# Kernel optimization log

Measured on AMD Instinct MI355X. Metric: run time of the kernel, lower is better.

## Reference

```python
import jax, jax.numpy as jnp
import numpy as np

N_II = 100000      # item nodes
N_UIU = 200000     # user + item nodes
D = 64             # embedding_dim
E_II = 600000
E_UIU = 1200000
L_II = 3           # num_layers_ii
L_UIU = 3          # num_layers_uiu
N_USERS = 100000   # items occupy indices [N_USERS, N_USERS+N_II)


def _lightgcn_embedding(x, edge_index, edge_weight, num_layers, num_nodes):
    """PyG LightGCN.get_embedding: symmetric gcn_norm (no self loops) + mean over layer outputs."""
    src, dst = edge_index[0], edge_index[1]
    # gcn_norm: deg over target nodes, weighted by edge_weight
    deg = jax.ops.segment_sum(edge_weight, dst, num_segments=num_nodes)
    deg_inv_sqrt = jnp.where(deg > 0, jax.lax.rsqrt(jnp.where(deg > 0, deg, 1.0)), 0.0)
    norm = deg_inv_sqrt[src] * edge_weight * deg_inv_sqrt[dst]  # [E]
    alpha = 1.0 / (num_layers + 1)
    out = x * alpha
    for _ in range(num_layers):
        # SpMM: gather source embeddings, scale, scatter-add to targets
        x = jax.ops.segment_sum(norm[:, None] * x[src], dst, num_segments=num_nodes)  # [N, D]
        out = out + x * alpha
    return out


def setup_inputs() -> dict:
    key = jax.random.key(0)
    k1, k2, k3, k4, k5, k6 = jax.random.split(key, 6)
    return {
        "emb_ii": jax.random.normal(k1, (N_II, D), dtype=jnp.float32),
        "emb_uiu": jax.random.normal(k2, (N_UIU, D), dtype=jnp.float32),
        "edge_attr_ii": jax.random.uniform(k3, (E_II,), dtype=jnp.float32),
        "edge_attr_uiu": jax.random.uniform(k4, (E_UIU,), dtype=jnp.float32),
        "edge_index_ii": jax.random.randint(k5, (2, E_II), 0, N_II, dtype=jnp.int32),
        "edge_index_uiu": jax.random.randint(k6, (2, E_UIU), 0, N_UIU, dtype=jnp.int32),
        # contiguous item block starting at N_USERS (node_mask_item.nonzero())
        "item_idx": jnp.arange(N_II, dtype=jnp.int32) + N_USERS,
    }


def reference(emb_ii, emb_uiu, edge_attr_ii, edge_attr_uiu,
              edge_index_ii, edge_index_uiu, item_idx):
    # item-item graph propagation
    h_ii = _lightgcn_embedding(emb_ii, edge_index_ii, edge_attr_ii, L_II, N_II)  # [N_II, D]
    # write item embeddings into the user-item embedding table
    emb_uiu = emb_uiu.at[item_idx].set(h_ii)
    # user-item graph propagation
    h_uiu = _lightgcn_embedding(emb_uiu, edge_index_uiu, edge_attr_uiu, L_UIU, N_UIU)  # [N_UIU, D]
    return h_uiu
```

## Files before the change

kernel.cpp:

```cpp
#include <hip/hip_runtime.h>


#define D       64
#define N_II    100000
#define N_UIU   200000
#define E_II    600000
#define E_UIU   1200000
#define N_USERS 100000
#define B       256
#define CR_K    8
#define FE_K    4

__device__ __forceinline__ unsigned short f2bf(float f) {
    unsigned u = __float_as_uint(f);
    u += 0x7fffu + ((u >> 16) & 1u);
    return (unsigned short)(u >> 16);
}
__device__ __forceinline__ void bf8_fma(float acc[8], uint4 p, float v) {
    acc[0] += v * __uint_as_float(p.x << 16);
    acc[1] += v * __uint_as_float(p.x & 0xffff0000u);
    acc[2] += v * __uint_as_float(p.y << 16);
    acc[3] += v * __uint_as_float(p.y & 0xffff0000u);
    acc[4] += v * __uint_as_float(p.z << 16);
    acc[5] += v * __uint_as_float(p.z & 0xffff0000u);
    acc[6] += v * __uint_as_float(p.w << 16);
    acc[7] += v * __uint_as_float(p.w & 0xffff0000u);
}
__device__ __forceinline__ void bf8_add(float acc[8], uint4 p) {
    acc[0] += __uint_as_float(p.x << 16);
    acc[1] += __uint_as_float(p.x & 0xffff0000u);
    acc[2] += __uint_as_float(p.y << 16);
    acc[3] += __uint_as_float(p.y & 0xffff0000u);
    acc[4] += __uint_as_float(p.z << 16);
    acc[5] += __uint_as_float(p.z & 0xffff0000u);
    acc[6] += __uint_as_float(p.w << 16);
    acc[7] += __uint_as_float(p.w & 0xffff0000u);
}
__device__ __forceinline__ uint4 pack8(const float a[8]) {
    uint4 r;
    r.x = (unsigned)f2bf(a[0]) | ((unsigned)f2bf(a[1]) << 16);
    r.y = (unsigned)f2bf(a[2]) | ((unsigned)f2bf(a[3]) << 16);
    r.z = (unsigned)f2bf(a[4]) | ((unsigned)f2bf(a[5]) << 16);
    r.w = (unsigned)f2bf(a[6]) | ((unsigned)f2bf(a[7]) << 16);
    return r;
}


__device__ __forceinline__ void rol_cnt(int bid, const int* __restrict__ dst,
                                        int* __restrict__ cnt, int* __restrict__ rank,
                                        int e0, int e1) {
    int base = e0 + bid * (B * CR_K) + threadIdx.x;
    int d[CR_K];
#pragma unroll
    for (int k = 0; k < CR_K; ++k) {
        int e = base + k * B;
        d[k] = (e < e1) ? dst[e] : 0;
    }
#pragma unroll
    for (int k = 0; k < CR_K; ++k) {
        int e = base + k * B;
        if (e < e1) rank[e] = atomicAdd(&cnt[d[k]], 1);
    }
}

__device__ __forceinline__ void rol_cvt(int bid, const float4* __restrict__ x,
                                        uint4* __restrict__ xb, int n8) {
    int i = bid * B + threadIdx.x;
    if (i >= n8) return;
    float4 a = x[2 * i], b = x[2 * i + 1];
    float t[8] = {a.x, a.y, a.z, a.w, b.x, b.y, b.z, b.w};
    xb[i] = pack8(t);
}

__device__ void rol_node(int bid, const int* __restrict__ cnt, int2* __restrict__ rr,
                         int* __restrict__ binrank, int* __restrict__ ghist,
                         int* __restrict__ gcur, int N) {
    __shared__ int sh[B];
    __shared__ int h[64], hb[64];
    __shared__ int sbase;
    int t = threadIdx.x;
    int i = bid * B + t;
    int c = (i < N) ? cnt[i] : 0;
    int b = (c < 63) ? c : 63;
    sh[t] = c;
    if (t < 64) h[t] = 0;
    __syncthreads();
    int rk = 0;
    if (i < N) rk = atomicAdd(&h[b], 1);
    for (int off = 1; off < B; off <<= 1) {
        int u = (t >= off) ? sh[t - off] : 0;
        __syncthreads();
        sh[t] += u;
        __syncthreads();
    }
    if (t == B - 1) sbase = atomicAdd(gcur, sh[B - 1]);
    if (t < 64) hb[t] = h[t] ? atomicAdd(&ghist[t], h[t]) : 0;
    __syncthreads();
    if (i < N) {
        int o = sbase + sh[t] - c;
        rr[i] = make_int2(o, o + c);
        binrank[i] = hb[b] + rk;
    }
}

__device__ __forceinline__ void rol_fillE(int bid, const int* __restrict__ src,
                                          const int* __restrict__ dst,
                                          const float* __restrict__ w,
                                          const int* __restrict__ rank,
                                          const int2* __restrict__ rr,
                                          int2* __restrict__ ev, int E) {
    int base = bid * (B * FE_K) + threadIdx.x;
    int d[FE_K], r[FE_K], s[FE_K];
    float ww[FE_K];
#pragma unroll
    for (int k = 0; k < FE_K; ++k) {
        int e = base + k * B;
        if (e < E) { d[k] = dst[e]; r[k] = rank[e]; s[k] = src[e]; ww[k] = w[e]; }
        else       { d[k] = 0; r[k] = 0; s[k] = 0; ww[k] = 0.f; }
    }
    int pos[FE_K];
#pragma unroll
    for (int k = 0; k < FE_K; ++k) pos[k] = rr[d[k]].x + r[k];
#pragma unroll
    for (int k = 0; k < FE_K; ++k) {
        int e = base + k * B;
        if (e < E) ev[pos[k]] = make_int2(s[k], __float_as_int(ww[k]));
    }
}

__device__ __forceinline__ void rol_deg(int bid, const int2* __restrict__ rr,
                                        const int2* __restrict__ ev,
                                        float* __restrict__ dis, int N) {
    int i = bid * B + threadIdx.x;
    if (i >= N) return;
    int2 se = rr[i];
    float dg = 0.f;
    for (int j = se.x; j < se.y; ++j) dg += __int_as_float(ev[j].y);
    dis[i] = (dg > 0.f) ? rsqrtf(dg) : 0.f;
}

__device__ void rol_valsc(int bid, const int2* __restrict__ rr, const float* __restrict__ dis,
                          const int* __restrict__ binrank, const int* __restrict__ ghist,
                          int2* __restrict__ ev, int* __restrict__ perm,
                          int2* __restrict__ rrp, int N) {
    __shared__ int sboff[64];
    int t = threadIdx.x;
    if (t < 64) {
        int v = ghist[t];
        int s = v;
        for (int o = 1; o < 64; o <<= 1) {
            int u = __shfl_up(s, o);
            if (t >= o) s += u;
        }
        sboff[t] = s - v;
    }
    __syncthreads();
    int i = bid * B + t;
    if (i >= N) return;
    int2 se = rr[i];
    float di = dis[i];
    for (int j = se.x; j < se.y; ++j) {
        int2 p = ev[j];
        ev[j].y = __float_as_int(di * __int_as_float(p.y) * dis[p.x]);
    }
    int c = se.y - se.x;
    int b = (c < 63) ? c : 63;
    int pos = sboff[b] + binrank[i];
    perm[pos] = i;
    rrp[pos]  = se;
}

__device__ void rol_spmm(int bid, const int2* __restrict__ rrp, const int* __restrict__ perm,
                         const int2* __restrict__ ev, const uint4* __restrict__ xb,
                         uint4* __restrict__ xn, int N) {
    int idx = bid * B + threadIdx.x;
    int vrow = idx >> 3;
    if (vrow >= N) return;
    int g = idx & 7;
    int2 se = rrp[vrow];
    int row = perm[vrow];
    float acc[8] = {0.f, 0.f, 0.f, 0.f, 0.f, 0.f, 0.f, 0.f};
    int j = se.x, e = se.y;
    for (; j + 3 < e; j += 4) {
        int2 p0 = ev[j], p1 = ev[j + 1], p2 = ev[j + 2], p3 = ev[j + 3];
        uint4 a0 = xb[p0.x * 8 + g];
        uint4 a1 = xb[p1.x * 8 + g];
        uint4 a2 = xb[p2.x * 8 + g];
        uint4 a3 = xb[p3.x * 8 + g];
        bf8_fma(acc, a0, __int_as_float(p0.y));
        bf8_fma(acc, a1, __int_as_float(p1.y));
        bf8_fma(acc, a2, __int_as_float(p2.y));
        bf8_fma(acc, a3, __int_as_float(p3.y));
    }
    for (; j < e; ++j) {
        int2 p0 = ev[j];
        uint4 a0 = xb[p0.x * 8 + g];
        bf8_fma(acc, a0, __int_as_float(p0.y));
    }
    xn[row * 8 + g] = pack8(acc);
}

__device__ void rol_final(int bid, const int2* __restrict__ rrp, const int* __restrict__ perm,
                          const int2* __restrict__ ev, const uint4* __restrict__ x2b,
                          const uint4* __restrict__ x1b, const uint4* __restrict__ x0b,
                          float4* __restrict__ out, uint4* __restrict__ outb,
                          float alpha, int N) {
    int idx = bid * B + threadIdx.x;
    int vrow = idx >> 3;
    if (vrow >= N) return;
    int g = idx & 7;
    int2 se = rrp[vrow];
    int row = perm[vrow];
    float acc[8] = {0.f, 0.f, 0.f, 0.f, 0.f, 0.f, 0.f, 0.f};
    int j = se.x, e = se.y;
    for (; j + 3 < e; j += 4) {
        int2 p0 = ev[j], p1 = ev[j + 1], p2 = ev[j + 2], p3 = ev[j + 3];
        uint4 a0 = x2b[p0.x * 8 + g];
        uint4 a1 = x2b[p1.x * 8 + g];
        uint4 a2 = x2b[p2.x * 8 + g];
        uint4 a3 = x2b[p3.x * 8 + g];
        bf8_fma(acc, a0, __int_as_float(p0.y));
        bf8_fma(acc, a1, __int_as_float(p1.y));
        bf8_fma(acc, a2, __int_as_float(p2.y));
        bf8_fma(acc, a3, __int_as_float(p3.y));
    }
    for (; j < e; ++j) {
        int2 p0 = ev[j];
        uint4 a0 = x2b[p0.x * 8 + g];
        bf8_fma(acc, a0, __int_as_float(p0.y));
    }
    bf8_add(acc, x1b[row * 8 + g]);
    bf8_add(acc, x2b[row * 8 + g]);
    bf8_add(acc, x0b[row * 8 + g]);
    float r[8];
#pragma unroll
    for (int k = 0; k < 8; ++k) r[k] = alpha * acc[k];
    if (out) {
        out[row * 16 + 2 * g]     = make_float4(r[0], r[1], r[2], r[3]);
        out[row * 16 + 2 * g + 1] = make_float4(r[4], r[5], r[6], r[7]);
    }
    if (outb) outb[row * 8 + g] = pack8(r);
}


__global__ void f_cnt_cvt2(int nbA, const int* dstA, int* cntA, int* rankA, int eA,
                           int nbB, const float4* xB, uint4* xbB, int n8B,
                           const float4* xC, uint4* xbC, int n8C) {
    int b = (int)blockIdx.x;
    if (b < nbA)       { rol_cnt(b, dstA, cntA, rankA, 0, eA); return; }
    b -= nbA;
    if (b < nbB)       { rol_cvt(b, xB, xbB, n8B); return; }
    rol_cvt(b - nbB, xC, xbC, n8C);
}

__global__ void f_node_cnt(int nbA, const int* cntN, int2* rr, int* brk, int* ghist,
                           int* gcur, int N,
                           const int* dstS, int* cntS, int* rankS, int e0, int e1) {
    int b = (int)blockIdx.x;
    if (b < nbA) rol_node(b, cntN, rr, brk, ghist, gcur, N);
    else         rol_cnt(b - nbA, dstS, cntS, rankS, e0, e1);
}

__global__ void f_fillE_cnt(int nbA, const int* src, const int* dst, const float* w,
                            const int* rank, const int2* rr, int2* ev, int E,
                            const int* dstS, int* cntS, int* rankS, int e0, int e1) {
    int b = (int)blockIdx.x;
    if (b < nbA) rol_fillE(b, src, dst, w, rank, rr, ev, E);
    else         rol_cnt(b - nbA, dstS, cntS, rankS, e0, e1);
}

__global__ void f_deg_cnt(int nbA, const int2* rr, const int2* ev, float* dis, int N,
                          const int* dstS, int* cntS, int* rankS, int e0, int e1) {
    int b = (int)blockIdx.x;
    if (b < nbA) rol_deg(b, rr, ev, dis, N);
    else         rol_cnt(b - nbA, dstS, cntS, rankS, e0, e1);
}

__global__ void f_valsc_cnt(int nbA, const int2* rr, const float* dis, const int* brk,
                            const int* ghist, int2* ev, int* perm, int2* rrp, int N,
                            const int* dstS, int* cntS, int* rankS, int e0, int e1) {
    int b = (int)blockIdx.x;
    if (b < nbA) rol_valsc(b, rr, dis, brk, ghist, ev, perm, rrp, N);
    else         rol_cnt(b - nbA, dstS, cntS, rankS, e0, e1);
}

__global__ void f_spmm_cnt(int nbA, const int2* rrp, const int* perm, const int2* ev,
                           const uint4* xb, uint4* xn, int N,
                           const int* dstS, int* cntS, int* rankS, int e0, int e1) {
    int b = (int)blockIdx.x;
    if (b < nbA) rol_spmm(b, rrp, perm, ev, xb, xn, N);
    else         rol_cnt(b - nbA, dstS, cntS, rankS, e0, e1);
}

__global__ void f_final_node(int nbA, const int2* rrpA, const int* permA, const int2* evA,
                             const uint4* x2b, const uint4* x1b, const uint4* x0b,
                             float4* outA, uint4* outbA, float alpha, int NA,
                             const int* cntN, int2* rrB, int* brkB, int* ghistB,
                             int* gcurB, int NB) {
    int b = (int)blockIdx.x;
    if (b < nbA) rol_final(b, rrpA, permA, evA, x2b, x1b, x0b, outA, outbA, alpha, NA);
    else         rol_node(b - nbA, cntN, rrB, brkB, ghistB, gcurB, NB);
}

__global__ void k_fillE(const int* src, const int* dst, const float* w, const int* rank,
                        const int2* rr, int2* ev, int E) {
    rol_fillE((int)blockIdx.x, src, dst, w, rank, rr, ev, E);
}
__global__ void k_deg(const int2* rr, const int2* ev, float* dis, int N) {
    rol_deg((int)blockIdx.x, rr, ev, dis, N);
}
__global__ void k_valsc(const int2* rr, const float* dis, const int* brk, const int* ghist,
                        int2* ev, int* perm, int2* rrp, int N) {
    rol_valsc((int)blockIdx.x, rr, dis, brk, ghist, ev, perm, rrp, N);
}
__global__ void k_spmm8(const int2* rrp, const int* perm, const int2* ev,
                        const uint4* xb, uint4* xn, int N) {
    rol_spmm((int)blockIdx.x, rrp, perm, ev, xb, xn, N);
}
__global__ void k_spmm8_final(const int2* rrp, const int* perm, const int2* ev,
                              const uint4* x2b, const uint4* x1b, const uint4* x0b,
                              float4* out, uint4* outb, float alpha, int N) {
    rol_final((int)blockIdx.x, rrp, perm, ev, x2b, x1b, x0b, out, outb, alpha, N);
}


static inline int nbx(int work, int per) { return (work + per - 1) / per; }

extern "C" void kernel_launch(void* const* d_in, const int* in_sizes, int n_in,
                              void* d_out, int out_size, void* d_ws, size_t ws_size,
                              hipStream_t stream) {
    const float* emb_ii  = (const float*)d_in[0];
    const float* emb_uiu = (const float*)d_in[1];
    const float* w_ii    = (const float*)d_in[2];
    const float* w_uiu   = (const float*)d_in[3];
    const int*   src_ii  = (const int*)d_in[4];
    const int*   dst_ii  = src_ii + E_II;
    const int*   src_uiu = (const int*)d_in[5];
    const int*   dst_uiu = src_uiu + E_UIU;
    float*       out     = (float*)d_out;

    uint4* xb0_u = (uint4*)d_ws;
    uint4* x1_u  = xb0_u + (size_t)N_UIU * 8;
    uint4* x2_u  = x1_u + (size_t)N_UIU * 8;

    int2*  ev1   = (int2*)(x2_u + (size_t)N_II * 8);
    int*   rank1 = (int*)(ev1 + E_II);
    int2*  rr1   = (int2*)(rank1 + E_II);
    int*   cnt1  = (int*)(rr1 + N_II);
    int*   gt1   = cnt1 + N_II;
    float* dis1  = (float*)(gt1 + 65);
    int*   brk1  = (int*)(dis1 + N_II);
    int*   perm1 = rank1;
    int2*  rrp1  = (int2*)(rank1 + N_II);

    int2*  ev2   = (int2*)(x2_u + (size_t)N_UIU * 8);
    int*   rank2 = (int*)(ev2 + E_UIU);
    int2*  rr2   = (int2*)(rank2 + E_UIU);
    int*   cnt2  = (int*)(rr2 + N_UIU);
    int*   gt2   = cnt2 + N_UIU;
    float* dis2  = (float*)(gt2 + 65);
    int*   brk2  = (int*)(dis2 + N_UIU);
    int*   perm2 = rank2;
    int2*  rrp2  = (int2*)(rank2 + N_UIU);

    uint4* g1_x0 = x1_u;
    uint4* g1_x1 = x1_u + (size_t)N_II * 8;
    uint4* g1_x2 = x2_u;
    uint4* hii_b = xb0_u + (size_t)N_USERS * 8;

    const float alpha = 0.25f;

    hipMemsetAsync(cnt1, 0, ((size_t)N_II + 65) * sizeof(int), stream);
    hipMemsetAsync(cnt2, 0, ((size_t)N_UIU + 65) * sizeof(int), stream);

    const int s[7] = {0, 128000, 320000, 448000, 640000, 920000, E_UIU};

    const int nbCnt1 = nbx(E_II, B * CR_K);
    const int nbCvt1 = nbx(N_II * 8, B);
    const int nbCvt2 = nbx(N_USERS * 8, B);
    const int nbN1   = nbx(N_II, B);
    const int nbF1   = nbx(E_II, B * FE_K);
    const int nbS1   = nbx(N_II * 8, B);
    const int nbN2   = nbx(N_UIU, B);
    const int nbF2   = nbx(E_UIU, B * FE_K);
    const int nbS2   = nbx(N_UIU * 8, B);

    f_cnt_cvt2<<<nbCnt1 + nbCvt1 + nbCvt2, B, 0, stream>>>(
        nbCnt1, dst_ii, cnt1, rank1, E_II,
        nbCvt1, (const float4*)emb_ii, g1_x0, N_II * 8,
        (const float4*)emb_uiu, xb0_u, N_USERS * 8);

    f_node_cnt<<<nbN1 + nbx(s[1] - s[0], B * CR_K), B, 0, stream>>>(
        nbN1, cnt1, rr1, brk1, gt1 + 1, gt1, N_II,
        dst_uiu, cnt2, rank2, s[0], s[1]);

    f_fillE_cnt<<<nbF1 + nbx(s[2] - s[1], B * CR_K), B, 0, stream>>>(
        nbF1, src_ii, dst_ii, w_ii, rank1, rr1, ev1, E_II,
        dst_uiu, cnt2, rank2, s[1], s[2]);

    f_deg_cnt<<<nbN1 + nbx(s[3] - s[2], B * CR_K), B, 0, stream>>>(
        nbN1, rr1, ev1, dis1, N_II,
        dst_uiu, cnt2, rank2, s[2], s[3]);

    f_valsc_cnt<<<nbN1 + nbx(s[4] - s[3], B * CR_K), B, 0, stream>>>(
        nbN1, rr1, dis1, brk1, gt1 + 1, ev1, perm1, rrp1, N_II,
        dst_uiu, cnt2, rank2, s[3], s[4]);

    f_spmm_cnt<<<nbS1 + nbx(s[5] - s[4], B * CR_K), B, 0, stream>>>(
        nbS1, rrp1, perm1, ev1, g1_x0, g1_x1, N_II,
        dst_uiu, cnt2, rank2, s[4], s[5]);

    f_spmm_cnt<<<nbS1 + nbx(s[6] - s[5], B * CR_K), B, 0, stream>>>(
        nbS1, rrp1, perm1, ev1, g1_x1, g1_x2, N_II,
        dst_uiu, cnt2, rank2, s[5], s[6]);

    f_final_node<<<nbS1 + nbN2, B, 0, stream>>>(
        nbS1, rrp1, perm1, ev1, g1_x2, g1_x1, g1_x0, nullptr, hii_b, alpha, N_II,
        cnt2, rr2, brk2, gt2 + 1, gt2, N_UIU);

    k_fillE<<<nbF2, B, 0, stream>>>(src_uiu, dst_uiu, w_uiu, rank2, rr2, ev2, E_UIU);
    k_deg  <<<nbN2, B, 0, stream>>>(rr2, ev2, dis2, N_UIU);
    k_valsc<<<nbN2, B, 0, stream>>>(rr2, dis2, brk2, gt2 + 1, ev2, perm2, rrp2, N_UIU);
    k_spmm8<<<nbS2, B, 0, stream>>>(rrp2, perm2, ev2, xb0_u, x1_u, N_UIU);
    k_spmm8<<<nbS2, B, 0, stream>>>(rrp2, perm2, ev2, x1_u, x2_u, N_UIU);
    k_spmm8_final<<<nbS2, B, 0, stream>>>(rrp2, perm2, ev2, x2_u, x1_u, xb0_u,
                                          (float4*)out, nullptr, alpha, N_UIU);
}
```

Before: 480.0 us.

## Store UIU embeddings in degree-sorted order and remap edge sources to sorted positions

The UIU graph's embedding tables are now stored in degree-bucket-sorted row order. Edge source indices are rewritten to sorted positions during normalization, so the SpMM passes read and write contiguous sorted rows without a perm indirection, and the original order is restored only when writing the final output. Kernel fusion is also reshuffled: counting is rebalanced into four chunks, node-prefix and fillE are merged into the item-graph SpMM launches, and conversion, degree and sort-finalization go into one mixed launch. This adds index remapping and a sortpos array in exchange for fewer launches and better locality, though the sorted layout may reduce gather locality compared with node order.

```diff
diff --git a/kernel.cpp b/kernel.cpp
--- a/kernel.cpp
+++ b/kernel.cpp
@@ -45,6 +45,21 @@
     return r;
 }
 
+__device__ __forceinline__ int bin_of(int c) { return (c < 63) ? c : 63; }
+
+__device__ __forceinline__ void scan_boff(const int* __restrict__ ghist, int* sboff) {
+    int t = threadIdx.x;
+    if (t < 64) {
+        int v = ghist[t];
+        int s = v;
+        for (int o = 1; o < 64; o <<= 1) {
+            int u = __shfl_up(s, o);
+            if (t >= o) s += u;
+        }
+        sboff[t] = s - v;
+    }
+}
+
 
 __device__ __forceinline__ void rol_cnt(int bid, const int* __restrict__ dst,
                                         int* __restrict__ cnt, int* __restrict__ rank,
@@ -81,7 +96,7 @@
     int t = threadIdx.x;
     int i = bid * B + t;
     int c = (i < N) ? cnt[i] : 0;
-    int b = (c < 63) ? c : 63;
+    int b = bin_of(c);
     sh[t] = c;
     if (t < 64) h[t] = 0;
     __syncthreads();
@@ -144,18 +159,9 @@
                           int2* __restrict__ ev, int* __restrict__ perm,
                           int2* __restrict__ rrp, int N) {
     __shared__ int sboff[64];
-    int t = threadIdx.x;
-    if (t < 64) {
-        int v = ghist[t];
-        int s = v;
-        for (int o = 1; o < 64; o <<= 1) {
-            int u = __shfl_up(s, o);
-            if (t >= o) s += u;
-        }
-        sboff[t] = s - v;
-    }
+    scan_boff(ghist, sboff);
     __syncthreads();
-    int i = bid * B + t;
+    int i = bid * B + threadIdx.x;
     if (i >= N) return;
     int2 se = rr[i];
     float di = dis[i];
@@ -163,11 +169,57 @@
         int2 p = ev[j];
         ev[j].y = __float_as_int(di * __int_as_float(p.y) * dis[p.x]);
     }
-    int c = se.y - se.x;
-    int b = (c < 63) ? c : 63;
-    int pos = sboff[b] + binrank[i];
+    int pos = sboff[bin_of(se.y - se.x)] + binrank[i];
     perm[pos] = i;
     rrp[pos]  = se;
+}
+
+__device__ void rol_sortfin(int bid, const int2* __restrict__ rr, const int* __restrict__ brk,
+                            const int* __restrict__ ghist, int* __restrict__ sortpos,
+                            int* __restrict__ perm, int2* __restrict__ srr, int N) {
+    __shared__ int sboff[64];
+    scan_boff(ghist, sboff);
+    __syncthreads();
+    int i = bid * B + threadIdx.x;
+    if (i >= N) return;
+    int2 se = rr[i];
+    int pos = sboff[bin_of(se.y - se.x)] + brk[i];
+    sortpos[i] = pos;
+    perm[pos] = i;
+    srr[pos]  = se;
+}
+
+__device__ __forceinline__ void rol_evnorm(int bid, const int2* __restrict__ rr,
+                                           const float* __restrict__ dis,
+                                           const int* __restrict__ sortpos,
+                                           int2* __restrict__ ev, int N) {
+    int i = bid * B + threadIdx.x;
+    if (i >= N) return;
+    int2 se = rr[i];
+    float di = dis[i];
+    for (int j = se.x; j < se.y; ++j) {
+        int2 p = ev[j];
+        ev[j] = make_int2(sortpos[p.x],
+                          __float_as_int(di * __int_as_float(p.y) * dis[p.x]));
+    }
+}
+
+__device__ void rol_cvts(int bid, const float4* __restrict__ xu,
+                         const int2* __restrict__ rr2, const int* __restrict__ brk2,
+                         const int* __restrict__ ghist2, uint4* __restrict__ xb0s,
+                         int Nrows) {
+    __shared__ int sboff[64];
+    scan_boff(ghist2, sboff);
+    __syncthreads();
+    int idx = bid * B + threadIdx.x;
+    int row = idx >> 3;
+    if (row >= Nrows) return;
+    int g = idx & 7;
+    int2 s2 = rr2[row];
+    int pos = sboff[bin_of(s2.y - s2.x)] + brk2[row];
+    float4 a = xu[(size_t)row * 16 + 2 * g], b = xu[(size_t)row * 16 + 2 * g + 1];
+    float t[8] = {a.x, a.y, a.z, a.w, b.x, b.y, b.z, b.w};
+    xb0s[(size_t)pos * 8 + g] = pack8(t);
 }
 
 __device__ void rol_spmm(int bid, const int2* __restrict__ rrp, const int* __restrict__ perm,
@@ -183,10 +235,10 @@
     int j = se.x, e = se.y;
     for (; j + 3 < e; j += 4) {
         int2 p0 = ev[j], p1 = ev[j + 1], p2 = ev[j + 2], p3 = ev[j + 3];
-        uint4 a0 = xb[p0.x * 8 + g];
-        uint4 a1 = xb[p1.x * 8 + g];
-        uint4 a2 = xb[p2.x * 8 + g];
-        uint4 a3 = xb[p3.x * 8 + g];
+        uint4 a0 = xb[(size_t)p0.x * 8 + g];
+        uint4 a1 = xb[(size_t)p1.x * 8 + g];
+        uint4 a2 = xb[(size_t)p2.x * 8 + g];
+        uint4 a3 = xb[(size_t)p3.x * 8 + g];
         bf8_fma(acc, a0, __int_as_float(p0.y));
         bf8_fma(acc, a1, __int_as_float(p1.y));
         bf8_fma(acc, a2, __int_as_float(p2.y));
@@ -194,17 +246,49 @@
     }
     for (; j < e; ++j) {
         int2 p0 = ev[j];
-        uint4 a0 = xb[p0.x * 8 + g];
-        bf8_fma(acc, a0, __int_as_float(p0.y));
-    }
-    xn[row * 8 + g] = pack8(acc);
-}
-
-__device__ void rol_final(int bid, const int2* __restrict__ rrp, const int* __restrict__ perm,
-                          const int2* __restrict__ ev, const uint4* __restrict__ x2b,
-                          const uint4* __restrict__ x1b, const uint4* __restrict__ x0b,
-                          float4* __restrict__ out, uint4* __restrict__ outb,
-                          float alpha, int N) {
+        uint4 a0 = xb[(size_t)p0.x * 8 + g];
+        bf8_fma(acc, a0, __int_as_float(p0.y));
+    }
+    xn[(size_t)row * 8 + g] = pack8(acc);
+}
+
+__device__ void rol_spmm_s(int bid, const int2* __restrict__ srr, const int2* __restrict__ ev,
+                           const uint4* __restrict__ xb, uint4* __restrict__ xn, int N) {
+    int idx = bid * B + threadIdx.x;
+    int vrow = idx >> 3;
+    if (vrow >= N) return;
+    int g = idx & 7;
+    int2 se = srr[vrow];
+    float acc[8] = {0.f, 0.f, 0.f, 0.f, 0.f, 0.f, 0.f, 0.f};
+    int j = se.x, e = se.y;
+    for (; j + 3 < e; j += 4) {
+        int2 p0 = ev[j], p1 = ev[j + 1], p2 = ev[j + 2], p3 = ev[j + 3];
+        uint4 a0 = xb[(size_t)p0.x * 8 + g];
+        uint4 a1 = xb[(size_t)p1.x * 8 + g];
+        uint4 a2 = xb[(size_t)p2.x * 8 + g];
+        uint4 a3 = xb[(size_t)p3.x * 8 + g];
+        bf8_fma(acc, a0, __int_as_float(p0.y));
+        bf8_fma(acc, a1, __int_as_float(p1.y));
+        bf8_fma(acc, a2, __int_as_float(p2.y));
+        bf8_fma(acc, a3, __int_as_float(p3.y));
+    }
+    for (; j < e; ++j) {
+        int2 p0 = ev[j];
+        uint4 a0 = xb[(size_t)p0.x * 8 + g];
+        bf8_fma(acc, a0, __int_as_float(p0.y));
+    }
+    xn[(size_t)vrow * 8 + g] = pack8(acc);
+}
+
+__device__ void rol_final1(int bid, const int2* __restrict__ rrp, const int* __restrict__ perm,
+                           const int2* __restrict__ ev, const uint4* __restrict__ x2b,
+                           const uint4* __restrict__ x1b, const uint4* __restrict__ x0b,
+                           const int2* __restrict__ rr2, const int* __restrict__ brk2,
+                           const int* __restrict__ ghist2, uint4* __restrict__ xb0s,
+                           float alpha, int N) {
+    __shared__ int sboff[64];
+    scan_boff(ghist2, sboff);
+    __syncthreads();
     int idx = bid * B + threadIdx.x;
     int vrow = idx >> 3;
     if (vrow >= N) return;
@@ -215,10 +299,10 @@
     int j = se.x, e = se.y;
     for (; j + 3 < e; j += 4) {
         int2 p0 = ev[j], p1 = ev[j + 1], p2 = ev[j + 2], p3 = ev[j + 3];
-        uint4 a0 = x2b[p0.x * 8 + g];
-        uint4 a1 = x2b[p1.x * 8 + g];
-        uint4 a2 = x2b[p2.x * 8 + g];
-        uint4 a3 = x2b[p3.x * 8 + g];
+        uint4 a0 = x2b[(size_t)p0.x * 8 + g];
+        uint4 a1 = x2b[(size_t)p1.x * 8 + g];
+        uint4 a2 = x2b[(size_t)p2.x * 8 + g];
+        uint4 a3 = x2b[(size_t)p3.x * 8 + g];
         bf8_fma(acc, a0, __int_as_float(p0.y));
         bf8_fma(acc, a1, __int_as_float(p1.y));
         bf8_fma(acc, a2, __int_as_float(p2.y));
@@ -226,31 +310,65 @@
     }
     for (; j < e; ++j) {
         int2 p0 = ev[j];
-        uint4 a0 = x2b[p0.x * 8 + g];
-        bf8_fma(acc, a0, __int_as_float(p0.y));
-    }
-    bf8_add(acc, x1b[row * 8 + g]);
-    bf8_add(acc, x2b[row * 8 + g]);
-    bf8_add(acc, x0b[row * 8 + g]);
+        uint4 a0 = x2b[(size_t)p0.x * 8 + g];
+        bf8_fma(acc, a0, __int_as_float(p0.y));
+    }
+    bf8_add(acc, x1b[(size_t)row * 8 + g]);
+    bf8_add(acc, x2b[(size_t)row * 8 + g]);
+    bf8_add(acc, x0b[(size_t)row * 8 + g]);
     float r[8];
 #pragma unroll
     for (int k = 0; k < 8; ++k) r[k] = alpha * acc[k];
-    if (out) {
-        out[row * 16 + 2 * g]     = make_float4(r[0], r[1], r[2], r[3]);
-        out[row * 16 + 2 * g + 1] = make_float4(r[4], r[5], r[6], r[7]);
-    }
-    if (outb) outb[row * 8 + g] = pack8(r);
-}
-
-
-__global__ void f_cnt_cvt2(int nbA, const int* dstA, int* cntA, int* rankA, int eA,
-                           int nbB, const float4* xB, uint4* xbB, int n8B,
-                           const float4* xC, uint4* xbC, int n8C) {
-    int b = (int)blockIdx.x;
-    if (b < nbA)       { rol_cnt(b, dstA, cntA, rankA, 0, eA); return; }
-    b -= nbA;
-    if (b < nbB)       { rol_cvt(b, xB, xbB, n8B); return; }
-    rol_cvt(b - nbB, xC, xbC, n8C);
+    int oi = N_USERS + row;
+    int2 s2 = rr2[oi];
+    int pos = sboff[bin_of(s2.y - s2.x)] + brk2[oi];
+    xb0s[(size_t)pos * 8 + g] = pack8(r);
+}
+
+__device__ void rol_final_s(int bid, const int2* __restrict__ srr, const int* __restrict__ perm,
+                            const int2* __restrict__ ev, const uint4* __restrict__ x2s,
+                            const uint4* __restrict__ x1s, const uint4* __restrict__ x0s,
+                            float4* __restrict__ out, float alpha, int N) {
+    int idx = bid * B + threadIdx.x;
+    int vrow = idx >> 3;
+    if (vrow >= N) return;
+    int g = idx & 7;
+    int2 se = srr[vrow];
+    float acc[8] = {0.f, 0.f, 0.f, 0.f, 0.f, 0.f, 0.f, 0.f};
+    int j = se.x, e = se.y;
+    for (; j + 3 < e; j += 4) {
+        int2 p0 = ev[j], p1 = ev[j + 1], p2 = ev[j + 2], p3 = ev[j + 3];
+        uint4 a0 = x2s[(size_t)p0.x * 8 + g];
+        uint4 a1 = x2s[(size_t)p1.x * 8 + g];
+        uint4 a2 = x2s[(size_t)p2.x * 8 + g];
+        uint4 a3 = x2s[(size_t)p3.x * 8 + g];
+        bf8_fma(acc, a0, __int_as_float(p0.y));
+        bf8_fma(acc, a1, __int_as_float(p1.y));
+        bf8_fma(acc, a2, __int_as_float(p2.y));
+        bf8_fma(acc, a3, __int_as_float(p3.y));
+    }
+    for (; j < e; ++j) {
+        int2 p0 = ev[j];
+        uint4 a0 = x2s[(size_t)p0.x * 8 + g];
+        bf8_fma(acc, a0, __int_as_float(p0.y));
+    }
+    bf8_add(acc, x1s[(size_t)vrow * 8 + g]);
+    bf8_add(acc, x2s[(size_t)vrow * 8 + g]);
+    bf8_add(acc, x0s[(size_t)vrow * 8 + g]);
+    float r[8];
+#pragma unroll
+    for (int k = 0; k < 8; ++k) r[k] = alpha * acc[k];
+    int orig = perm[vrow];
+    out[(size_t)orig * 16 + 2 * g]     = make_float4(r[0], r[1], r[2], r[3]);
+    out[(size_t)orig * 16 + 2 * g + 1] = make_float4(r[4], r[5], r[6], r[7]);
+}
+
+
+__global__ void f_cnt_cvt(int nbA, const int* dstA, int* cntA, int* rankA, int eA,
+                          const float4* xB, uint4* xbB, int n8B) {
+    int b = (int)blockIdx.x;
+    if (b < nbA) rol_cnt(b, dstA, cntA, rankA, 0, eA);
+    else         rol_cvt(b - nbA, xB, xbB, n8B);
 }
 
 __global__ void f_node_cnt(int nbA, const int* cntN, int2* rr, int* brk, int* ghist,
@@ -284,47 +402,57 @@
     else         rol_cnt(b - nbA, dstS, cntS, rankS, e0, e1);
 }
 
-__global__ void f_spmm_cnt(int nbA, const int2* rrp, const int* perm, const int2* ev,
-                           const uint4* xb, uint4* xn, int N,
-                           const int* dstS, int* cntS, int* rankS, int e0, int e1) {
-    int b = (int)blockIdx.x;
-    if (b < nbA) rol_spmm(b, rrp, perm, ev, xb, xn, N);
-    else         rol_cnt(b - nbA, dstS, cntS, rankS, e0, e1);
-}
-
-__global__ void f_final_node(int nbA, const int2* rrpA, const int* permA, const int2* evA,
-                             const uint4* x2b, const uint4* x1b, const uint4* x0b,
-                             float4* outA, uint4* outbA, float alpha, int NA,
-                             const int* cntN, int2* rrB, int* brkB, int* ghistB,
-                             int* gcurB, int NB) {
-    int b = (int)blockIdx.x;
-    if (b < nbA) rol_final(b, rrpA, permA, evA, x2b, x1b, x0b, outA, outbA, alpha, NA);
+__global__ void f_spmm_node(int nbA, const int2* rrp, const int* perm, const int2* ev,
+                            const uint4* xb, uint4* xn, int NA,
+                            const int* cntN, int2* rrB, int* brkB, int* ghistB,
+                            int* gcurB, int NB) {
+    int b = (int)blockIdx.x;
+    if (b < nbA) rol_spmm(b, rrp, perm, ev, xb, xn, NA);
     else         rol_node(b - nbA, cntN, rrB, brkB, ghistB, gcurB, NB);
 }
 
-__global__ void k_fillE(const int* src, const int* dst, const float* w, const int* rank,
-                        const int2* rr, int2* ev, int E) {
-    rol_fillE((int)blockIdx.x, src, dst, w, rank, rr, ev, E);
-}
-__global__ void k_deg(const int2* rr, const int2* ev, float* dis, int N) {
-    rol_deg((int)blockIdx.x, rr, ev, dis, N);
-}
-__global__ void k_valsc(const int2* rr, const float* dis, const int* brk, const int* ghist,
-                        int2* ev, int* perm, int2* rrp, int N) {
-    rol_valsc((int)blockIdx.x, rr, dis, brk, ghist, ev, perm, rrp, N);
-}
-__global__ void k_spmm8(const int2* rrp, const int* perm, const int2* ev,
-                        const uint4* xb, uint4* xn, int N) {
-    rol_spmm((int)blockIdx.x, rrp, perm, ev, xb, xn, N);
-}
-__global__ void k_spmm8_final(const int2* rrp, const int* perm, const int2* ev,
-                              const uint4* x2b, const uint4* x1b, const uint4* x0b,
-                              float4* out, uint4* outb, float alpha, int N) {
-    rol_final((int)blockIdx.x, rrp, perm, ev, x2b, x1b, x0b, out, outb, alpha, N);
-}
-
-
-static inline int nbx(int work, int per) { return (work + per - 1) / per; }
+__global__ void f_spmm_fill(int nbA, const int2* rrp, const int* perm, const int2* ev,
+                            const uint4* xb, uint4* xn, int NA,
+                            const int* srcB, const int* dstB, const float* wB,
+                            const int* rankB, const int2* rrB, int2* evB, int EB) {
+    int b = (int)blockIdx.x;
+    if (b < nbA) rol_spmm(b, rrp, perm, ev, xb, xn, NA);
+    else         rol_fillE(b - nbA, srcB, dstB, wB, rankB, rrB, evB, EB);
+}
+
+__global__ void f_final_mix(int nbA, const int2* rrp1, const int* perm1, const int2* ev1,
+                            const uint4* x2b, const uint4* x1b, const uint4* x0b,
+                            float alpha, int N1,
+                            int nbB, const float4* xu,
+                            int nbC, const int2* rr2, const int2* ev2, float* dis2, int N2,
+                            const int* brk2, const int* ghist2, uint4* xb0s,
+                            int* sortpos2, int* perm2, int2* srr2) {
+    int b = (int)blockIdx.x;
+    if (b < nbA) { rol_final1(b, rrp1, perm1, ev1, x2b, x1b, x0b,
+                              rr2, brk2, ghist2, xb0s, alpha, N1); return; }
+    b -= nbA;
+    if (b < nbB) { rol_cvts(b, xu, rr2, brk2, ghist2, xb0s, N_USERS); return; }
+    b -= nbB;
+    if (b < nbC) { rol_deg(b, rr2, ev2, dis2, N2); return; }
+    rol_sortfin(b - nbC, rr2, brk2, ghist2, sortpos2, perm2, srr2, N2);
+}
+
+__global__ void k_evnorm(const int2* rr, const float* dis, const int* sortpos,
+                         int2* ev, int N) {
+    rol_evnorm((int)blockIdx.x, rr, dis, sortpos, ev, N);
+}
+__global__ void k_spmm_s(const int2* srr, const int2* ev, const uint4* xb,
+                         uint4* xn, int N) {
+    rol_spmm_s((int)blockIdx.x, srr, ev, xb, xn, N);
+}
+__global__ void k_final_s(const int2* srr, const int* perm, const int2* ev,
+                          const uint4* x2s, const uint4* x1s, const uint4* x0s,
+                          float4* out, float alpha, int N) {
+    rol_final_s((int)blockIdx.x, srr, perm, ev, x2s, x1s, x0s, out, alpha, N);
+}
+
+
+static inline int nbx(long long work, int per) { return (int)((work + per - 1) / per); }
 
 extern "C" void kernel_launch(void* const* d_in, const int* in_sizes, int n_in,
                               void* d_out, int out_size, void* d_ws, size_t ws_size,
@@ -355,40 +483,39 @@
 
     int2*  ev2   = (int2*)(x2_u + (size_t)N_UIU * 8);
     int*   rank2 = (int*)(ev2 + E_UIU);
+    int*   perm2 = rank2;
+    int2*  srr2  = (int2*)(rank2 + N_UIU);
     int2*  rr2   = (int2*)(rank2 + E_UIU);
     int*   cnt2  = (int*)(rr2 + N_UIU);
+    int*   sortpos2 = cnt2;
     int*   gt2   = cnt2 + N_UIU;
-    float* dis2  = (float*)(gt2 + 65);
-    int*   brk2  = (int*)(dis2 + N_UIU);
-    int*   perm2 = rank2;
-    int2*  rrp2  = (int2*)(rank2 + N_UIU);
+    int*   brk2  = gt2 + 65;
+    float* dis2  = (float*)(brk2 + N_UIU);
 
     uint4* g1_x0 = x1_u;
     uint4* g1_x1 = x1_u + (size_t)N_II * 8;
     uint4* g1_x2 = x2_u;
-    uint4* hii_b = xb0_u + (size_t)N_USERS * 8;
 
     const float alpha = 0.25f;
 
     hipMemsetAsync(cnt1, 0, ((size_t)N_II + 65) * sizeof(int), stream);
     hipMemsetAsync(cnt2, 0, ((size_t)N_UIU + 65) * sizeof(int), stream);
 
-    const int s[7] = {0, 128000, 320000, 448000, 640000, 920000, E_UIU};
+    const int s[5] = {0, 300000, 600000, 900000, E_UIU};
 
     const int nbCnt1 = nbx(E_II, B * CR_K);
-    const int nbCvt1 = nbx(N_II * 8, B);
-    const int nbCvt2 = nbx(N_USERS * 8, B);
+    const int nbCvt1 = nbx((long long)N_II * 8, B);
     const int nbN1   = nbx(N_II, B);
     const int nbF1   = nbx(E_II, B * FE_K);
-    const int nbS1   = nbx(N_II * 8, B);
+    const int nbS1   = nbx((long long)N_II * 8, B);
     const int nbN2   = nbx(N_UIU, B);
     const int nbF2   = nbx(E_UIU, B * FE_K);
-    const int nbS2   = nbx(N_UIU * 8, B);
-
-    f_cnt_cvt2<<<nbCnt1 + nbCvt1 + nbCvt2, B, 0, stream>>>(
+    const int nbS2   = nbx((long long)N_UIU * 8, B);
+    const int nbCvt2 = nbx((long long)N_USERS * 8, B);
+
+    f_cnt_cvt<<<nbCnt1 + nbCvt1, B, 0, stream>>>(
         nbCnt1, dst_ii, cnt1, rank1, E_II,
-        nbCvt1, (const float4*)emb_ii, g1_x0, N_II * 8,
-        (const float4*)emb_uiu, xb0_u, N_USERS * 8);
+        (const float4*)emb_ii, g1_x0, N_II * 8);
 
     f_node_cnt<<<nbN1 + nbx(s[1] - s[0], B * CR_K), B, 0, stream>>>(
         nbN1, cnt1, rr1, brk1, gt1 + 1, gt1, N_II,
@@ -406,23 +533,24 @@
         nbN1, rr1, dis1, brk1, gt1 + 1, ev1, perm1, rrp1, N_II,
         dst_uiu, cnt2, rank2, s[3], s[4]);
 
-    f_spmm_cnt<<<nbS1 + nbx(s[5] - s[4], B * CR_K), B, 0, stream>>>(
+    f_spmm_node<<<nbS1 + nbN2, B, 0, stream>>>(
         nbS1, rrp1, perm1, ev1, g1_x0, g1_x1, N_II,
-        dst_uiu, cnt2, rank2, s[4], s[5]);
-
-    f_spmm_cnt<<<nbS1 + nbx(s[6] - s[5], B * CR_K), B, 0, stream>>>(
+        cnt2, rr2, brk2, gt2 + 1, gt2, N_UIU);
+
+    f_spmm_fill<<<nbS1 + nbF2, B, 0, stream>>>(
         nbS1, rrp1, perm1, ev1, g1_x1, g1_x2, N_II,
-        dst_uiu, cnt2, rank2, s[5], s[6]);
-
-    f_final_node<<<nbS1 + nbN2, B, 0, stream>>>(
-        nbS1, rrp1, perm1, ev1, g1_x2, g1_x1, g1_x0, nullptr, hii_b, alpha, N_II,
-        cnt2, rr2, brk2, gt2 + 1, gt2, N_UIU);
-
-    k_fillE<<<nbF2, B, 0, stream>>>(src_uiu, dst_uiu, w_uiu, rank2, rr2, ev2, E_UIU);
-    k_deg  <<<nbN2, B, 0, stream>>>(rr2, ev2, dis2, N_UIU);
-    k_valsc<<<nbN2, B, 0, stream>>>(rr2, dis2, brk2, gt2 + 1, ev2, perm2, rrp2, N_UIU);
-    k_spmm8<<<nbS2, B, 0, stream>>>(rrp2, perm2, ev2, xb0_u, x1_u, N_UIU);
-    k_spmm8<<<nbS2, B, 0, stream>>>(rrp2, perm2, ev2, x1_u, x2_u, N_UIU);
-    k_spmm8_final<<<nbS2, B, 0, stream>>>(rrp2, perm2, ev2, x2_u, x1_u, xb0_u,
-                                          (float4*)out, nullptr, alpha, N_UIU);
-}
+        src_uiu, dst_uiu, w_uiu, rank2, rr2, ev2, E_UIU);
+
+    f_final_mix<<<nbS1 + nbCvt2 + nbN2 + nbN2, B, 0, stream>>>(
+        nbS1, rrp1, perm1, ev1, g1_x2, g1_x1, g1_x0, alpha, N_II,
+        nbCvt2, (const float4*)emb_uiu,
+        nbN2, rr2, ev2, dis2, N_UIU,
+        brk2, gt2 + 1, xb0_u, sortpos2, perm2, srr2);
+
+    k_evnorm<<<nbN2, B, 0, stream>>>(rr2, dis2, sortpos2, ev2, N_UIU);
+
+    k_spmm_s<<<nbS2, B, 0, stream>>>(srr2, ev2, xb0_u, x1_u, N_UIU);
+    k_spmm_s<<<nbS2, B, 0, stream>>>(srr2, ev2, x1_u, x2_u, N_UIU);
+    k_final_s<<<nbS2, B, 0, stream>>>(srr2, perm2, ev2, x2_u, x1_u, xb0_u,
+                                      (float4*)out, alpha, N_UIU);
+}
```

After: 486.7 us. About the same (+1.4%).
